# Performance work log

Measured on AMD Instinct MI355X. Metric: run time of the kernel, lower is better.

Reference implementation:

```python
import jax, jax.numpy as jnp
import numpy as np
import math

N = 20000          # nodes
E = 320000         # edges (avg degree 16)
NS, NV = 16, 4     # scalar / vector multiplicities
NCAT = 10
CAT_VOCAB = 119
DIST_DIM = 32
LIG_MAX_R = 5.0
W1_NUMEL = NS * NS + NS * NV          # 320 : layer1 tp weights
W2_NUMEL = NS * NS + NV * NS + NS * NV + NV * NV + NV * NV  # 416


def setup_inputs() -> dict:
    key = jax.random.key(0)
    ks = jax.random.split(key, 24)
    s = 0.1
    inp = {
        'x_cat': jax.random.randint(ks[0], (N, NCAT), 0, 2),
        'x_scalar': jax.random.normal(ks[1], (N, 32), jnp.float32),
        'pos': jax.random.normal(ks[2], (N, 3), jnp.float32) * 3.0,
        'edge_index': jax.random.randint(ks[3], (2, E), 0, N),
        'edge_bond': jax.random.uniform(ks[4], (E, 10), jnp.float32),
        # AtomEncoder params
        'emb_tables': jax.random.normal(ks[5], (NCAT, CAT_VOCAB, NS)) * s,
        'node_w': jax.random.normal(ks[6], (32, NS)) * s,
        'node_b': jnp.zeros((NS,), jnp.float32),
        # lig_edge_embedding MLP (42 -> ns -> ns)
        'em_w1': jax.random.normal(ks[7], (10 + DIST_DIM, NS)) * s,
        'em_b1': jnp.zeros((NS,), jnp.float32),
        'em_w2': jax.random.normal(ks[8], (NS, NS)) * s,
        'em_b2': jnp.zeros((NS,), jnp.float32),
        'c1_w1': jax.random.normal(ks[9], (3 * NS, 3 * NS)) * s,
        'c1_b1': jnp.zeros((3 * NS,), jnp.float32),
        'c1_w2': jax.random.normal(ks[10], (3 * NS, W1_NUMEL)) * s,
        'c1_b2': jnp.zeros((W1_NUMEL,), jnp.float32),
        # conv layer 2 fc
        'c2_w1': jax.random.normal(ks[11], (3 * NS, 3 * NS)) * s,
        'c2_b1': jnp.zeros((3 * NS,), jnp.float32),
        'c2_w2': jax.random.normal(ks[12], (3 * NS, W2_NUMEL)) * s,
        'c2_b2': jnp.zeros((W2_NUMEL,), jnp.float32),
    }
    return inp


def _scatter_mean(vals, idx, n):
    s = jax.ops.segment_sum(vals, idx, num_segments=n)
    cnt = jax.ops.segment_sum(jnp.ones(idx.shape, vals.dtype), idx, num_segments=n)
    return s / jnp.maximum(cnt, 1.0)[:, None]


def _forward(x_cat, x_scalar, pos, edge_index, edge_bond,
             emb_tables, node_w, node_b, em_w1, em_b1, em_w2, em_b2,
             c1_w1, c1_b1, c1_w2, c1_b2, c2_w1, c2_b1, c2_w2, c2_b2):
    ns, nv = NS, NV
    n = x_cat.shape[0]
    # ---- AtomEncoder: sum of categorical embeddings + linear(scalar) ----
    gathered = emb_tables[jnp.arange(NCAT)[None, :], x_cat]      # [N, 10, ns]
    node = gathered.sum(axis=1) + x_scalar @ node_w + node_b    # [N, ns]

    src, dst = edge_index[0], edge_index[1]
    vec = pos[dst] - pos[src]                                   # [E, 3]
    dist = jnp.sqrt(jnp.sum(vec * vec, axis=-1) + 1e-12)
    unit = vec / (dist + 1e-8)[:, None]
    # spherical harmonics, lmax=1, component normalization: [1, sqrt(3)*r_hat]
    sh0 = jnp.ones((vec.shape[0], 1), vec.dtype)
    sh1 = math.sqrt(3.0) * unit                                 # [E, 3]

    # ---- GaussianSmearing + edge embedding MLP ----
    offset = jnp.linspace(0.0, LIG_MAX_R, DIST_DIM)
    coeff = -0.5 / float(LIG_MAX_R / (DIST_DIM - 1)) ** 2
    demb = jnp.exp(coeff * (dist[:, None] - offset[None, :]) ** 2)
    e_in = jnp.concatenate([edge_bond, demb], axis=1)           # [E, 42]
    edge_emb = jax.nn.relu(e_in @ em_w1 + em_b1) @ em_w2 + em_b2  # [E, ns]

    # ======== conv layer 1: ns x0e -> ns x0e + nv x1o ========
    ea = jnp.concatenate([edge_emb, node[src, :ns], node[dst, :ns]], axis=1)
    w = jax.nn.relu(ea @ c1_w1 + c1_b1) @ c1_w2 + c1_b2         # [E, 320]
    wa = w[:, :ns * ns].reshape(-1, ns, ns)
    wb = w[:, ns * ns:].reshape(-1, ns, nv)
    s_dst = node[dst]                                           # [E, ns]
    a = 1.0 / math.sqrt(ns)                                     # fan-in norm
    out0 = jnp.einsum('euk,eu->ek', wa, s_dst) * sh0 * a        # 0e x 0e -> 0e
    out1 = jnp.einsum('euw,eu->ew', wb, s_dst)[:, :, None] * sh1[:, None, :] * a
    tp = jnp.concatenate([out0, out1.reshape(-1, 3 * nv)], axis=1)
    node = _scatter_mean(tp, src, n)                            # [N, ns+3nv]

    # ======== conv layer 2: ns x0e + nv x1o -> ns x0e + nv x1o + nv x1e ====
    ea = jnp.concatenate([edge_emb, node[src, :ns], node[dst, :ns]], axis=1)
    w = jax.nn.relu(ea @ c2_w1 + c2_b1) @ c2_w2 + c2_b2         # [E, 416]
    o = 0
    wa = w[:, o:o + ns * ns].reshape(-1, ns, ns); o += ns * ns
    wb = w[:, o:o + nv * ns].reshape(-1, nv, ns); o += nv * ns
    wc = w[:, o:o + ns * nv].reshape(-1, ns, nv); o += ns * nv
    wd = w[:, o:o + nv * nv].reshape(-1, nv, nv); o += nv * nv
    we = w[:, o:o + nv * nv].reshape(-1, nv, nv)
    s = node[dst, :ns]
    v = node[dst, ns:].reshape(-1, nv, 3)
    a0 = 1.0 / math.sqrt(ns + nv)   # two paths into 0e
    a1 = 1.0 / math.sqrt(ns + nv)   # two paths into 1o
    aE = 1.0 / math.sqrt(nv)        # one path into 1e
    vdot = jnp.einsum('evi,ei->ev', v, sh1)                     # 1o . 1o
    out0 = (jnp.einsum('euk,eu->ek', wa, s) * sh0
            + jnp.einsum('euk,eu->ek', wb, vdot) / math.sqrt(3.0)) * a0
    out1o = (jnp.einsum('euw,eu->ew', wc, s)[:, :, None] * sh1[:, None, :]
             + jnp.einsum('euw,eui->ewi', wd, v) * sh0[:, :, None]) * a1
    crossv = jnp.cross(v, jnp.broadcast_to(sh1[:, None, :], v.shape))
    out1e = jnp.einsum('euw,eui->ewi', we, crossv) * (aE / math.sqrt(2.0))
    tp = jnp.concatenate([out0, out1o.reshape(-1, 3 * nv),
                          out1e.reshape(-1, 3 * nv)], axis=1)
    node = _scatter_mean(tp, src, n)                            # [N, ns+6nv] = [N,40]
    return node


def reference(x_cat, x_scalar, pos, edge_index, edge_bond,
              emb_tables, node_w, node_b, em_w1, em_b1, em_w2, em_b2,
              c1_w1, c1_b1, c1_w2, c1_b2, c2_w1, c2_b1, c2_w2, c2_b2):
    return _forward(x_cat, x_scalar, pos, edge_index, edge_bond,
                    emb_tables, node_w, node_b, em_w1, em_b1, em_w2, em_b2,
                    c1_w1, c1_b1, c1_w2, c1_b2, c2_w1, c2_b1, c2_w2, c2_b2)
```

## Files before the change

kernel.cpp:

```cpp
#include <hip/hip_runtime.h>
#include <math.h>

#define NN 20000
#define NE 320000
#define NCPY 4

typedef _Float16 f16x8 __attribute__((ext_vector_type(8)));
typedef float f32x4 __attribute__((ext_vector_type(4)));
typedef unsigned short ushort_t;
typedef unsigned int uint_t;

#define MFMA16(A,B,C) __builtin_amdgcn_mfma_f32_16x16x32_f16((A),(B),(C),0,0,0)
#define LDS_FENCE() do{ asm volatile("s_waitcnt lgkmcnt(0)" ::: "memory"); __builtin_amdgcn_sched_barrier(0);}while(0)

static_assert(NE % 256 == 0, "edge grid must tile exactly");

__device__ __forceinline__ float frelu(float x){ return fmaxf(x, 0.0f); }

__device__ __forceinline__ void splitf(float x, ushort_t& h, ushort_t& l){
    _Float16 hh = (_Float16)x;
    float r = (x - (float)hh) * 2048.0f;
    _Float16 ll = (_Float16)r;
    union { _Float16 f; ushort_t u; } ch, cl;
    ch.f = hh; cl.f = ll;
    h = ch.u; l = cl.u;
}

__device__ __forceinline__ void edge_embed(
    int e, int s, int d,
    const float* __restrict__ pos,
    const float* __restrict__ edge_bond,
    const float* __restrict__ em_w1, const float* __restrict__ em_b1,
    const float* __restrict__ em_w2, const float* __restrict__ em_b2,
    float* eemb, float* sh1)
{
    float vx = pos[d*3+0] - pos[s*3+0];
    float vy = pos[d*3+1] - pos[s*3+1];
    float vz = pos[d*3+2] - pos[s*3+2];
    float d2 = vx*vx + vy*vy + vz*vz + 1e-12f;
    float dist = sqrtf(d2);
    float inv = 1.0f / (dist + 1e-8f);
    const float SQ3 = 1.7320508075688772f;
    sh1[0] = SQ3 * vx * inv;
    sh1[1] = SQ3 * vy * inv;
    sh1[2] = SQ3 * vz * inv;

    float ein[42];
    #pragma unroll
    for (int t = 0; t < 10; ++t) ein[t] = edge_bond[e*10 + t];
    const float coeff = -19.22f;
    const float step  = 5.0f / 31.0f;
    #pragma unroll
    for (int k = 0; k < 32; ++k) {
        float dd = dist - step * (float)k;
        ein[10+k] = __expf(coeff * dd * dd);
    }

    float t1[16];
    #pragma unroll
    for (int j = 0; j < 16; ++j) t1[j] = em_b1[j];
    #pragma unroll
    for (int t = 0; t < 42; ++t) {
        float v = ein[t];
        #pragma unroll
        for (int j = 0; j < 16; ++j) t1[j] += v * em_w1[t*16 + j];
    }
    #pragma unroll
    for (int j = 0; j < 16; ++j) t1[j] = frelu(t1[j]);

    #pragma unroll
    for (int j = 0; j < 16; ++j) eemb[j] = em_b2[j];
    #pragma unroll
    for (int t = 0; t < 16; ++t) {
        float v = t1[t];
        #pragma unroll
        for (int j = 0; j < 16; ++j) eemb[j] += v * em_w2[t*16 + j];
    }
}

__global__ __launch_bounds__(256)
void k_node_y(const float* __restrict__ node, int stride,
              const float* __restrict__ w1, float* __restrict__ y)
{
    int n = blockIdx.x*256 + threadIdx.x;
    if (n >= NN) return;
    float sv[16];
    const float4* r = reinterpret_cast<const float4*>(node + (size_t)n*stride);
    #pragma unroll
    for (int k = 0; k < 4; ++k) {
        float4 q = r[k];
        sv[4*k]=q.x; sv[4*k+1]=q.y; sv[4*k+2]=q.z; sv[4*k+3]=q.w;
    }
    float yb[48];
    #pragma unroll
    for (int j = 0; j < 48; ++j) yb[j] = 0.f;
    #pragma unroll
    for (int t = 0; t < 16; ++t) {
        float v = sv[t];
        #pragma unroll
        for (int j = 0; j < 48; ++j) yb[j] += v * w1[(16+t)*48 + j];
    }
    float* yo = y + (size_t)n*96;
    #pragma unroll
    for (int j = 0; j < 12; ++j)
        reinterpret_cast<float4*>(yo)[j] = make_float4(yb[4*j], yb[4*j+1], yb[4*j+2], yb[4*j+3]);
    #pragma unroll
    for (int j = 0; j < 48; ++j) yb[j] = 0.f;
    #pragma unroll
    for (int t = 0; t < 16; ++t) {
        float v = sv[t];
        #pragma unroll
        for (int j = 0; j < 48; ++j) yb[j] += v * w1[(32+t)*48 + j];
    }
    #pragma unroll
    for (int j = 0; j < 12; ++j)
        reinterpret_cast<float4*>(yo + 48)[j] = make_float4(yb[4*j], yb[4*j+1], yb[4*j+2], yb[4*j+3]);
}

__global__ __launch_bounds__(256)
void k_pack(const float* __restrict__ w2, const float* __restrict__ b2,
            ushort_t* __restrict__ out, int NC, int ntiles)
{
    int slot = blockIdx.x*256 + threadIdx.x;
    if (slot >= ntiles*128) return;
    int tl = slot >> 7; int r7 = slot & 127; int kb = r7 >> 6; int ll = r7 & 63;
    int col = tl*16 + (ll & 15);
    int k0 = (kb<<5) + ((ll>>4)<<3);
    uint_t hw[4], lw[4];
    #pragma unroll
    for (int p = 0; p < 4; ++p) {
        int ka = k0 + 2*p, kb2 = k0 + 2*p + 1;
        float va = (ka < 48) ? w2[ka*NC + col] : (ka == 48 ? b2[col] : 0.0f);
        float vb = (kb2 < 48) ? w2[kb2*NC + col] : (kb2 == 48 ? b2[col] : 0.0f);
        ushort_t ah, al, bh, bl;
        splitf(va, ah, al);
        splitf(vb, bh, bl);
        hw[p] = (uint_t)ah | ((uint_t)bh << 16);
        lw[p] = (uint_t)al | ((uint_t)bl << 16);
    }
    int base = tl*2048 + kb*1024 + ll*8;
    *reinterpret_cast<uint4*>(&out[base])       = make_uint4(hw[0], hw[1], hw[2], hw[3]);
    *reinterpret_cast<uint4*>(&out[base + 512]) = make_uint4(lw[0], lw[1], lw[2], lw[3]);
}

struct B4 { f16x8 h0, l0, h1, l1; };
__device__ __forceinline__ B4 loadB(const f16x8* __restrict__ g, int t, int l) {
    B4 b;
    const f16x8* p = g + t*256 + l;
    b.h0 = p[0];
    b.l0 = p[64];
    b.h1 = p[128];
    b.l1 = p[192];
    return b;
}

__device__ __forceinline__ void stage_A(ushort_t* bounce, int l,
                                        const uint_t* hph, const uint_t* hpl,
                                        f16x8 ahi[4][2], f16x8 alo[4][2])
{
    #pragma unroll
    for (int t = 0; t < 4; ++t)
        *reinterpret_cast<uint4*>(&bounce[l*32 + t*8]) = make_uint4(0,0,0,0);
    LDS_FENCE();
    #pragma unroll
    for (int mt = 0; mt < 4; ++mt) {
        if ((l >> 4) == mt) {
            #pragma unroll
            for (int jj = 0; jj < 25; ++jj) {
                int k = jj*2, kb = k >> 5, kk = k & 31;
                int lr = (l & 15) + ((kk >> 3) << 4);
                int off = kb*512 + lr*8 + (kk & 7);
                *reinterpret_cast<uint_t*>(&bounce[off])        = hph[jj];
                *reinterpret_cast<uint_t*>(&bounce[1024 + off]) = hpl[jj];
            }
        }
        LDS_FENCE();
        ahi[mt][0] = *reinterpret_cast<const f16x8*>(&bounce[l*8]);
        ahi[mt][1] = *reinterpret_cast<const f16x8*>(&bounce[512 + l*8]);
        alo[mt][0] = *reinterpret_cast<const f16x8*>(&bounce[1024 + l*8]);
        alo[mt][1] = *reinterpret_cast<const f16x8*>(&bounce[1536 + l*8]);
        LDS_FENCE();
    }
}

__device__ __forceinline__ void build_h_reg(
    const float* em, int s, int d,
    const float* __restrict__ y,
    const float* __restrict__ w1, const float* __restrict__ b1,
    float* h)
{
    #pragma unroll
    for (int j = 0; j < 48; ++j) h[j] = b1[j];
    #pragma unroll
    for (int t = 0; t < 16; ++t) {
        float v = em[t];
        #pragma unroll
        for (int j = 0; j < 48; ++j) h[j] += v * w1[t*48 + j];
    }
    const float4* pb = reinterpret_cast<const float4*>(y + (size_t)s*96);
    const float4* pc = reinterpret_cast<const float4*>(y + (size_t)d*96 + 48);
    #pragma unroll
    for (int kk = 0; kk < 12; ++kk) {
        float4 qb = pb[kk], qc = pc[kk];
        h[4*kk+0] = frelu(h[4*kk+0] + qb.x + qc.x);
        h[4*kk+1] = frelu(h[4*kk+1] + qb.y + qc.y);
        h[4*kk+2] = frelu(h[4*kk+2] + qb.z + qc.z);
        h[4*kk+3] = frelu(h[4*kk+3] + qb.w + qc.w);
    }
}

__global__ __launch_bounds__(256)
void k_node_feat(const int* __restrict__ x_cat, const float* __restrict__ x_scalar,
                 const float* __restrict__ emb, const float* __restrict__ node_w,
                 const float* __restrict__ node_b, float* __restrict__ node0)
{
    int n = blockIdx.x * 256 + threadIdx.x;
    if (n >= NN) return;
    float acc[16];
    #pragma unroll
    for (int k = 0; k < 16; ++k) acc[k] = node_b[k];
    #pragma unroll
    for (int c = 0; c < 10; ++c) {
        int idx = x_cat[n*10 + c];
        const float4* row = reinterpret_cast<const float4*>(emb + (c*119 + idx)*16);
        #pragma unroll
        for (int k = 0; k < 4; ++k) {
            float4 q = row[k];
            acc[4*k+0] += q.x; acc[4*k+1] += q.y; acc[4*k+2] += q.z; acc[4*k+3] += q.w;
        }
    }
    #pragma unroll
    for (int t = 0; t < 32; ++t) {
        float xs = x_scalar[n*32 + t];
        #pragma unroll
        for (int k = 0; k < 16; ++k) acc[k] += xs * node_w[t*16 + k];
    }
    #pragma unroll
    for (int k = 0; k < 16; ++k) node0[n*16 + k] = acc[k];
}

__global__ __launch_bounds__(256)
void k_edge_l1(const int* __restrict__ ei, const float* __restrict__ pos,
               const float* __restrict__ edge_bond,
               const float* __restrict__ em_w1, const float* __restrict__ em_b1,
               const float* __restrict__ em_w2, const float* __restrict__ em_b2,
               const float* __restrict__ w1, const float* __restrict__ b1,
               const ushort_t* __restrict__ packW,
               const float* __restrict__ y,
               const float* __restrict__ node0,
               float* __restrict__ eembG, float* __restrict__ eshG,
               float* __restrict__ accumC, float* __restrict__ cnt)
{
    __shared__ __align__(16) unsigned char smem[20736];
    float* sT  = (float*)smem;
    float* sSh = (float*)(smem + 16640);
    int*   sSrc= (int*)(smem + 19712);

    int tid = threadIdx.x;
    int l = tid & 63;
    int cc = l & 15;
    int e = blockIdx.x*256 + tid;
    int s = ei[e], d = ei[NE + e];
    float* __restrict__ accum = accumC + (size_t)(blockIdx.x & (NCPY-1)) * (NN*28);

    float em[16], sh1[3];
    edge_embed(e, s, d, pos, edge_bond, em_w1, em_b1, em_w2, em_b2, em, sh1);
    {
        float4* pe = reinterpret_cast<float4*>(eembG + (size_t)e*16);
        #pragma unroll
        for (int k = 0; k < 4; ++k)
            pe[k] = make_float4(em[4*k], em[4*k+1], em[4*k+2], em[4*k+3]);
        reinterpret_cast<float4*>(eshG)[e] = make_float4(sh1[0], sh1[1], sh1[2], 0.f);
    }
    atomicAdd(cnt + s, 1.0f);

    float sd[16];
    {
        const float4* rd = reinterpret_cast<const float4*>(node0 + (size_t)d*16);
        #pragma unroll
        for (int k = 0; k < 4; ++k) {
            float4 q = rd[k];
            sd[4*k]=q.x; sd[4*k+1]=q.y; sd[4*k+2]=q.z; sd[4*k+3]=q.w;
        }
    }
    float h[48];
    build_h_reg(em, s, d, y, w1, b1, h);

    uint_t hph[25], hpl[25];
    #pragma unroll
    for (int jj = 0; jj < 24; ++jj) {
        ushort_t ah, al, bh, bl;
        splitf(h[2*jj],   ah, al);
        splitf(h[2*jj+1], bh, bl);
        hph[jj] = (uint_t)ah | ((uint_t)bh << 16);
        hpl[jj] = (uint_t)al | ((uint_t)bl << 16);
    }
    hph[24] = 0x3C00u;
    hpl[24] = 0u;

    f16x8 ahi[4][2], alo[4][2];
    stage_A((ushort_t*)smem + (tid >> 6)*2048, l, hph, hpl, ahi, alo);

    __syncthreads();
    sSrc[tid] = s;
    #pragma unroll
    for (int u = 0; u < 16; ++u) sT[u*260 + tid] = sd[u];
    sSh[tid*3+0] = sh1[0]; sSh[tid*3+1] = sh1[1]; sSh[tid*3+2] = sh1[2];
    __syncthreads();

    f32x4 out0[4];
    float ob[4][4];
    #pragma unroll
    for (int mt = 0; mt < 4; ++mt) {
        out0[mt] = (f32x4){0.f,0.f,0.f,0.f};
        #pragma unroll
        for (int r = 0; r < 4; ++r) ob[mt][r] = 0.f;
    }

    const f16x8* gB = reinterpret_cast<const f16x8*>(packW);

    auto process = [&](int t, const B4& cur) {
        #pragma unroll
        for (int mt = 0; mt < 4; ++mt) {
            f32x4 Dh = (f32x4){0.f,0.f,0.f,0.f};
            f32x4 Dc = (f32x4){0.f,0.f,0.f,0.f};
            Dh = MFMA16(ahi[mt][0], cur.h0, Dh);
            Dh = MFMA16(ahi[mt][1], cur.h1, Dh);
            Dc = MFMA16(alo[mt][0], cur.h0, Dc);
            Dc = MFMA16(ahi[mt][0], cur.l0, Dc);
            Dc = MFMA16(alo[mt][1], cur.h1, Dc);
            Dc = MFMA16(ahi[mt][1], cur.l1, Dc);
            f32x4 D = Dh + Dc * 0.00048828125f;
            int elb = (tid & 192) + (mt << 4) + ((l >> 4) << 2);
            if (t < 16) {
                f32x4 sv = *reinterpret_cast<const f32x4*>(&sT[t*260 + elb]);
                out0[mt] += sv * D;
            } else {
                const float* sp = &sT[(((t-16)<<2) + (cc>>2))*260 + elb];
                #pragma unroll
                for (int r = 0; r < 4; ++r) ob[mt][r] += sp[r] * D[r];
            }
        }
    };

    B4 b0 = loadB(gB, 0, l), b1v = loadB(gB, 1, l);
    #pragma unroll 1
    for (int t = 0; t < 20; t += 2) {
        B4 p0 = (t + 2 < 20) ? loadB(gB, t + 2, l) : b0;
        process(t, b0);
        B4 p1 = (t + 3 < 20) ? loadB(gB, t + 3, l) : b1v;
        process(t + 1, b1v);
        b0 = p0; b1v = p1;
    }

    #pragma unroll
    for (int mt = 0; mt < 4; ++mt) {
        int elb = (tid & 192) + (mt << 4) + ((l >> 4) << 2);
        #pragma unroll
        for (int r = 0; r < 4; ++r) {
            int el = elb + r;
            int sidx = sSrc[el];
            atomicAdd(accum + (size_t)sidx*28 + cc, out0[mt][r] * 0.25f);
            float x = ob[mt][r];
            x += __shfl_xor(x, 4); x += __shfl_xor(x, 8);
            int q = cc / 3; int i = cc - q*3;
            float xq = __shfl(x, (l & 48) | q);
            if (cc < 12)
                atomicAdd(accum + (size_t)sidx*28 + 16 + cc, 0.25f * xq * sSh[el*3 + i]);
        }
    }
}

__global__ __launch_bounds__(256)
void k_edge_l2(const int* __restrict__ ei,
               const float* __restrict__ w1, const float* __restrict__ b1,
               const ushort_t* __restrict__ packW,
               const float* __restrict__ eembG, const float* __restrict__ eshG,
               const float* __restrict__ y,
               const float* __restrict__ node1,
               float* __restrict__ accumC)
{
    __shared__ __align__(16) unsigned char smem[37376];
    float* sT  = (float*)smem;
    float* sVd = (float*)(smem + 16640);
    float* sV  = (float*)(smem + 20800);
    float* sSh = (float*)(smem + 33280);
    int*   sSrc= (int*)(smem + 36352);

    int tid = threadIdx.x;
    int l = tid & 63;
    int cc = l & 15;
    int e = blockIdx.x*256 + tid;
    int s = ei[e], d = ei[NE + e];
    float* __restrict__ accum2 = accumC + (size_t)(blockIdx.x & (NCPY-1)) * (NN*40);

    float4 shv = reinterpret_cast<const float4*>(eshG)[e];
    float sh1[3] = {shv.x, shv.y, shv.z};
    float sd[16], vv[12];
    {
        const float4* rd = reinterpret_cast<const float4*>(node1 + (size_t)d*28);
        #pragma unroll
        for (int k = 0; k < 4; ++k) {
            float4 q = rd[k];
            sd[4*k]=q.x; sd[4*k+1]=q.y; sd[4*k+2]=q.z; sd[4*k+3]=q.w;
        }
        #pragma unroll
        for (int k = 0; k < 3; ++k) {
            float4 q = rd[4+k];
            vv[4*k]=q.x; vv[4*k+1]=q.y; vv[4*k+2]=q.z; vv[4*k+3]=q.w;
        }
    }
    float vdr[4];
    const float INV_SQ3 = 0.5773502691896258f;
    #pragma unroll
    for (int u = 0; u < 4; ++u)
        vdr[u] = (vv[u*3]*sh1[0] + vv[u*3+1]*sh1[1] + vv[u*3+2]*sh1[2]) * INV_SQ3;

    float em[16];
    {
        const float4* pe = reinterpret_cast<const float4*>(eembG + (size_t)e*16);
        #pragma unroll
        for (int k = 0; k < 4; ++k) {
            float4 q = pe[k];
            em[4*k]=q.x; em[4*k+1]=q.y; em[4*k+2]=q.z; em[4*k+3]=q.w;
        }
    }
    float h[48];
    build_h_reg(em, s, d, y, w1, b1, h);

    uint_t hph[25], hpl[25];
    #pragma unroll
    for (int jj = 0; jj < 24; ++jj) {
        ushort_t ah, al, bh, bl;
        splitf(h[2*jj],   ah, al);
        splitf(h[2*jj+1], bh, bl);
        hph[jj] = (uint_t)ah | ((uint_t)bh << 16);
        hpl[jj] = (uint_t)al | ((uint_t)bl << 16);
    }
    hph[24] = 0x3C00u;
    hpl[24] = 0u;

    f16x8 ahi[4][2], alo[4][2];
    stage_A((ushort_t*)smem + (tid >> 6)*2048, l, hph, hpl, ahi, alo);

    __syncthreads();
    sSrc[tid] = s;
    #pragma unroll
    for (int u = 0; u < 16; ++u) sT[u*260 + tid] = sd[u];
    #pragma unroll
    for (int u = 0; u < 4; ++u) sVd[u*260 + tid] = vdr[u];
    #pragma unroll
    for (int k = 0; k < 12; ++k) sV[k*260 + tid] = vv[k];
    sSh[tid*3+0] = sh1[0]; sSh[tid*3+1] = sh1[1]; sSh[tid*3+2] = sh1[2];
    __syncthreads();

    const float A0 = 0.22360679774997896f;
    const float AE = 0.3535533905932738f;

    f32x4 out0[4];
    float outc[4][4];
    #pragma unroll
    for (int mt = 0; mt < 4; ++mt) {
        out0[mt] = (f32x4){0.f,0.f,0.f,0.f};
        #pragma unroll
        for (int r = 0; r < 4; ++r) outc[mt][r] = 0.f;
    }

    const f16x8* gB = reinterpret_cast<const f16x8*>(packW);

    auto process = [&](int t, const B4& cur) {
        #pragma unroll
        for (int mt = 0; mt < 4; ++mt) {
            f32x4 Dh = (f32x4){0.f,0.f,0.f,0.f};
            f32x4 Dc = (f32x4){0.f,0.f,0.f,0.f};
            Dh = MFMA16(ahi[mt][0], cur.h0, Dh);
            Dh = MFMA16(ahi[mt][1], cur.h1, Dh);
            Dc = MFMA16(alo[mt][0], cur.h0, Dc);
            Dc = MFMA16(ahi[mt][0], cur.l0, Dc);
            Dc = MFMA16(alo[mt][1], cur.h1, Dc);
            Dc = MFMA16(ahi[mt][1], cur.l1, Dc);
            f32x4 D = Dh + Dc * 0.00048828125f;
            int elb = (tid & 192) + (mt << 4) + ((l >> 4) << 2);
            if (t < 16) {
                f32x4 sv = *reinterpret_cast<const f32x4*>(&sT[t*260 + elb]);
                out0[mt] += sv * D;
            } else if (t < 20) {
                f32x4 vd = *reinterpret_cast<const f32x4*>(&sVd[(t-16)*260 + elb]);
                out0[mt] += vd * D;
            } else if (t < 24) {
                const float* sp = &sT[(((t-20)<<2) + (cc>>2))*260 + elb];
                #pragma unroll
                for (int r = 0; r < 4; ++r) outc[mt][r] += sp[r] * D[r];
            } else if (t == 24) {
                int base3 = (cc >> 2) * 3;
                #pragma unroll
                for (int r = 0; r < 4; ++r) {
                    int el = elb + r;
                    float vx = sV[(base3+0)*260 + el];
                    float vy = sV[(base3+1)*260 + el];
                    float vz = sV[(base3+2)*260 + el];
                    float a0 = D[r]*vx, a1 = D[r]*vy, a2 = D[r]*vz;
                    a0 += __shfl_xor(a0,4); a0 += __shfl_xor(a0,8);
                    a1 += __shfl_xor(a1,4); a1 += __shfl_xor(a1,8);
                    a2 += __shfl_xor(a2,4); a2 += __shfl_xor(a2,8);
                    float xc = outc[mt][r];
                    xc += __shfl_xor(xc,4); xc += __shfl_xor(xc,8);
                    int q = cc / 3; int i = cc - q*3;
                    int srcl = (l & 48) | q;
                    float g0 = __shfl(a0, srcl), g1 = __shfl(a1, srcl), g2 = __shfl(a2, srcl);
                    float oo = (i==0) ? g0 : ((i==1) ? g1 : g2);
                    float xq = __shfl(xc, srcl);
                    if (cc < 12) {
                        float sh1i = sSh[el*3 + i];
                        atomicAdd(accum2 + (size_t)sSrc[el]*40 + 16 + cc,
                                  A0 * (xq * sh1i + oo));
                    }
                }
            } else {
                int base3 = (cc >> 2) * 3;
                #pragma unroll
                for (int r = 0; r < 4; ++r) {
                    int el = elb + r;
                    float vx = sV[(base3+0)*260 + el];
                    float vy = sV[(base3+1)*260 + el];
                    float vz = sV[(base3+2)*260 + el];
                    float sx = sSh[el*3+0], sy = sSh[el*3+1], sz = sSh[el*3+2];
                    float cx = vy*sz - vz*sy;
                    float cy = vz*sx - vx*sz;
                    float cz = vx*sy - vy*sx;
                    float a0 = D[r]*cx, a1 = D[r]*cy, a2 = D[r]*cz;
                    a0 += __shfl_xor(a0,4); a0 += __shfl_xor(a0,8);
                    a1 += __shfl_xor(a1,4); a1 += __shfl_xor(a1,8);
                    a2 += __shfl_xor(a2,4); a2 += __shfl_xor(a2,8);
                    int q = cc / 3; int i = cc - q*3;
                    int srcl = (l & 48) | q;
                    float g0 = __shfl(a0, srcl), g1 = __shfl(a1, srcl), g2 = __shfl(a2, srcl);
                    float oo = (i==0) ? g0 : ((i==1) ? g1 : g2);
                    if (cc < 12)
                        atomicAdd(accum2 + (size_t)sSrc[el]*40 + 28 + cc, AE * oo);
                }
            }
        }
    };

    B4 b0 = loadB(gB, 0, l), b1v = loadB(gB, 1, l);
    #pragma unroll 1
    for (int t = 0; t < 26; t += 2) {
        B4 p0 = (t + 2 < 26) ? loadB(gB, t + 2, l) : b0;
        process(t, b0);
        B4 p1 = (t + 3 < 26) ? loadB(gB, t + 3, l) : b1v;
        process(t + 1, b1v);
        b0 = p0; b1v = p1;
    }

    #pragma unroll
    for (int mt = 0; mt < 4; ++mt) {
        int elb = (tid & 192) + (mt << 4) + ((l >> 4) << 2);
        #pragma unroll
        for (int r = 0; r < 4; ++r) {
            int el = elb + r;
            atomicAdd(accum2 + (size_t)sSrc[el]*40 + cc, out0[mt][r] * A0);
        }
    }
}

__global__ __launch_bounds__(256)
void k_divm(const float* __restrict__ in, int stride, float* __restrict__ out,
            const float* __restrict__ cnt, int cols, int total)
{
    int i = blockIdx.x * 256 + threadIdx.x;
    if (i >= total) return;
    int n = i / cols;
    float sum = 0.f;
    #pragma unroll
    for (int c = 0; c < NCPY; ++c) sum += in[(size_t)c*stride + i];
    out[i] = sum / fmaxf(cnt[n], 1.0f);
}

extern "C" void kernel_launch(void* const* d_in, const int* in_sizes, int n_in,
                              void* d_out, int out_size, void* d_ws, size_t ws_size,
                              hipStream_t stream) {
    const int*   x_cat     = (const int*)  d_in[0];
    const float* x_scalar  = (const float*)d_in[1];
    const float* pos       = (const float*)d_in[2];
    const int*   ei        = (const int*)  d_in[3];
    const float* edge_bond = (const float*)d_in[4];
    const float* emb       = (const float*)d_in[5];
    const float* node_w    = (const float*)d_in[6];
    const float* node_b    = (const float*)d_in[7];
    const float* em_w1     = (const float*)d_in[8];
    const float* em_b1     = (const float*)d_in[9];
    const float* em_w2     = (const float*)d_in[10];
    const float* em_b2     = (const float*)d_in[11];
    const float* c1_w1     = (const float*)d_in[12];
    const float* c1_b1     = (const float*)d_in[13];
    const float* c1_w2     = (const float*)d_in[14];
    const float* c1_b2     = (const float*)d_in[15];
    const float* c2_w1     = (const float*)d_in[16];
    const float* c2_b1     = (const float*)d_in[17];
    const float* c2_w2     = (const float*)d_in[18];
    const float* c2_b2     = (const float*)d_in[19];

    float* ws    = (float*)d_ws;
    float* node0 = ws;
    float* cnt   = ws + 320000;
    ushort_t* packA = (ushort_t*)(ws + 340000);
    ushort_t* packB = packA + 20*2048;
    float* eembG = ws + 400000;
    float* eshG  = ws + 5520000;
    float* yBuf  = ws + 6800000;
    float* node1 = ws + 8720000;
    float* accumC= ws + 9280000;

    hipMemsetAsync(cnt, 0, 20000 * sizeof(float), stream);
    hipMemsetAsync(accumC, 0, (size_t)NCPY * NN * 28 * sizeof(float), stream);

    k_pack<<<(20*128 + 255) / 256, 256, 0, stream>>>(c1_w2, c1_b2, packA, 320, 20);
    k_pack<<<(26*128 + 255) / 256, 256, 0, stream>>>(c2_w2, c2_b2, packB, 416, 26);

    k_node_feat<<<(NN + 255) / 256, 256, 0, stream>>>(
        x_cat, x_scalar, emb, node_w, node_b, node0);

    k_node_y<<<(NN + 255) / 256, 256, 0, stream>>>(node0, 16, c1_w1, yBuf);

    k_edge_l1<<<NE / 256, 256, 0, stream>>>(
        ei, pos, edge_bond, em_w1, em_b1, em_w2, em_b2,
        c1_w1, c1_b1, packA, yBuf, node0, eembG, eshG, accumC, cnt);

    k_divm<<<(560000 + 255) / 256, 256, 0, stream>>>(accumC, NN*28, node1, cnt, 28, 560000);

    hipMemsetAsync(accumC, 0, (size_t)NCPY * NN * 40 * sizeof(float), stream);

    k_node_y<<<(NN + 255) / 256, 256, 0, stream>>>(node1, 28, c2_w1, yBuf);

    k_edge_l2<<<NE / 256, 256, 0, stream>>>(
        ei, c2_w1, c2_b1, packB, eembG, eshG, yBuf, node1, accumC);

    k_divm<<<(800000 + 255) / 256, 256, 0, stream>>>(accumC, NN*40, (float*)d_out, cnt, 40, 800000);
}
```

Baseline: 333.2 us.

## Replace atomic scatter-mean with CSR sort by source and segmented gather

Builds a CSR ordering of edges by source node (degree count, single-block scan, atomic scatter into a permutation). The edge kernels then process edges in that sorted order and write per-edge tensor-product rows densely instead of doing float atomics into four replicated accumulators. A gather kernel sums each node's contiguous rows and divides by degree. This removes atomic contention and the memsets and reduction passes, but adds three preprocessing kernels (one a single-block serial scan), a large per-edge intermediate buffer, and indirect, less coalesced edge input reads through perm.

```diff
diff --git a/kernel.cpp b/kernel.cpp
--- a/kernel.cpp
+++ b/kernel.cpp
@@ -3,7 +3,6 @@
 
 #define NN 20000
 #define NE 320000
-#define NCPY 4
 
 typedef _Float16 f16x8 __attribute__((ext_vector_type(8)));
 typedef float f32x4 __attribute__((ext_vector_type(4)));
@@ -79,6 +78,47 @@
 }
 
 __global__ __launch_bounds__(256)
+void k_deg(const int* __restrict__ ei, int* __restrict__ deg)
+{
+    int e = blockIdx.x*256 + threadIdx.x;
+    if (e < NE) atomicAdd(&deg[ei[e]], 1);
+}
+
+__global__ __launch_bounds__(256)
+void k_scan(const int* __restrict__ deg, int* __restrict__ rowptr, int* __restrict__ off)
+{
+    __shared__ int part[256];
+    int t = threadIdx.x;
+    const int chunk = (NN + 255) / 256;
+    int lo = t*chunk, hi = lo + chunk; if (hi > NN) hi = NN; if (lo > NN) lo = NN;
+    int s = 0;
+    for (int i = lo; i < hi; ++i) s += deg[i];
+    part[t] = s;
+    __syncthreads();
+    for (int ofs = 1; ofs < 256; ofs <<= 1) {
+        int v = (t >= ofs) ? part[t-ofs] : 0;
+        __syncthreads();
+        part[t] += v;
+        __syncthreads();
+    }
+    int run = (t == 0) ? 0 : part[t-1];
+    for (int i = lo; i < hi; ++i) {
+        rowptr[i] = run; off[i] = run;
+        run += deg[i];
+    }
+    if (t == 255) rowptr[NN] = NE;
+}
+
+__global__ __launch_bounds__(256)
+void k_scatter(const int* __restrict__ ei, int* __restrict__ off, int* __restrict__ perm)
+{
+    int e = blockIdx.x*256 + threadIdx.x;
+    if (e >= NE) return;
+    int p = atomicAdd(&off[ei[e]], 1);
+    perm[p] = e;
+}
+
+__global__ __launch_bounds__(256)
 void k_node_y(const float* __restrict__ node, int stride,
               const float* __restrict__ w1, float* __restrict__ y)
 {
@@ -248,31 +288,31 @@
                const ushort_t* __restrict__ packW,
                const float* __restrict__ y,
                const float* __restrict__ node0,
+               const int* __restrict__ perm,
                float* __restrict__ eembG, float* __restrict__ eshG,
-               float* __restrict__ accumC, float* __restrict__ cnt)
+               float* __restrict__ tp)
 {
     __shared__ __align__(16) unsigned char smem[20736];
     float* sT  = (float*)smem;
     float* sSh = (float*)(smem + 16640);
-    int*   sSrc= (int*)(smem + 19712);
 
     int tid = threadIdx.x;
     int l = tid & 63;
     int cc = l & 15;
-    int e = blockIdx.x*256 + tid;
+    int i = blockIdx.x*256 + tid;
+    int e = perm[i];
     int s = ei[e], d = ei[NE + e];
-    float* __restrict__ accum = accumC + (size_t)(blockIdx.x & (NCPY-1)) * (NN*28);
+    size_t rowbase = (size_t)blockIdx.x * 256;
 
     float em[16], sh1[3];
     edge_embed(e, s, d, pos, edge_bond, em_w1, em_b1, em_w2, em_b2, em, sh1);
     {
-        float4* pe = reinterpret_cast<float4*>(eembG + (size_t)e*16);
+        float4* pe = reinterpret_cast<float4*>(eembG + (size_t)i*16);
         #pragma unroll
         for (int k = 0; k < 4; ++k)
             pe[k] = make_float4(em[4*k], em[4*k+1], em[4*k+2], em[4*k+3]);
-        reinterpret_cast<float4*>(eshG)[e] = make_float4(sh1[0], sh1[1], sh1[2], 0.f);
-    }
-    atomicAdd(cnt + s, 1.0f);
+        reinterpret_cast<float4*>(eshG)[i] = make_float4(sh1[0], sh1[1], sh1[2], 0.f);
+    }
 
     float sd[16];
     {
@@ -302,7 +342,6 @@
     stage_A((ushort_t*)smem + (tid >> 6)*2048, l, hph, hpl, ahi, alo);
 
     __syncthreads();
-    sSrc[tid] = s;
     #pragma unroll
     for (int u = 0; u < 16; ++u) sT[u*260 + tid] = sd[u];
     sSh[tid*3+0] = sh1[0]; sSh[tid*3+1] = sh1[1]; sSh[tid*3+2] = sh1[2];
@@ -359,14 +398,14 @@
         #pragma unroll
         for (int r = 0; r < 4; ++r) {
             int el = elb + r;
-            int sidx = sSrc[el];
-            atomicAdd(accum + (size_t)sidx*28 + cc, out0[mt][r] * 0.25f);
+            float* row = tp + (rowbase + el)*28;
+            row[cc] = out0[mt][r] * 0.25f;
             float x = ob[mt][r];
             x += __shfl_xor(x, 4); x += __shfl_xor(x, 8);
-            int q = cc / 3; int i = cc - q*3;
+            int q = cc / 3; int i2 = cc - q*3;
             float xq = __shfl(x, (l & 48) | q);
             if (cc < 12)
-                atomicAdd(accum + (size_t)sidx*28 + 16 + cc, 0.25f * xq * sSh[el*3 + i]);
+                row[16 + cc] = 0.25f * xq * sSh[el*3 + i2];
         }
     }
 }
@@ -378,23 +417,24 @@
                const float* __restrict__ eembG, const float* __restrict__ eshG,
                const float* __restrict__ y,
                const float* __restrict__ node1,
-               float* __restrict__ accumC)
-{
-    __shared__ __align__(16) unsigned char smem[37376];
+               const int* __restrict__ perm,
+               float* __restrict__ tp)
+{
+    __shared__ __align__(16) unsigned char smem[36352];
     float* sT  = (float*)smem;
     float* sVd = (float*)(smem + 16640);
     float* sV  = (float*)(smem + 20800);
     float* sSh = (float*)(smem + 33280);
-    int*   sSrc= (int*)(smem + 36352);
 
     int tid = threadIdx.x;
     int l = tid & 63;
     int cc = l & 15;
-    int e = blockIdx.x*256 + tid;
+    int i = blockIdx.x*256 + tid;
+    int e = perm[i];
     int s = ei[e], d = ei[NE + e];
-    float* __restrict__ accum2 = accumC + (size_t)(blockIdx.x & (NCPY-1)) * (NN*40);
-
-    float4 shv = reinterpret_cast<const float4*>(eshG)[e];
+    size_t rowbase = (size_t)blockIdx.x * 256;
+
+    float4 shv = reinterpret_cast<const float4*>(eshG)[i];
     float sh1[3] = {shv.x, shv.y, shv.z};
     float sd[16], vv[12];
     {
@@ -418,7 +458,7 @@
 
     float em[16];
     {
-        const float4* pe = reinterpret_cast<const float4*>(eembG + (size_t)e*16);
+        const float4* pe = reinterpret_cast<const float4*>(eembG + (size_t)i*16);
         #pragma unroll
         for (int k = 0; k < 4; ++k) {
             float4 q = pe[k];
@@ -444,7 +484,6 @@
     stage_A((ushort_t*)smem + (tid >> 6)*2048, l, hph, hpl, ahi, alo);
 
     __syncthreads();
-    sSrc[tid] = s;
     #pragma unroll
     for (int u = 0; u < 16; ++u) sT[u*260 + tid] = sd[u];
     #pragma unroll
@@ -505,15 +544,14 @@
                     a2 += __shfl_xor(a2,4); a2 += __shfl_xor(a2,8);
                     float xc = outc[mt][r];
                     xc += __shfl_xor(xc,4); xc += __shfl_xor(xc,8);
-                    int q = cc / 3; int i = cc - q*3;
+                    int q = cc / 3; int i2 = cc - q*3;
                     int srcl = (l & 48) | q;
                     float g0 = __shfl(a0, srcl), g1 = __shfl(a1, srcl), g2 = __shfl(a2, srcl);
-                    float oo = (i==0) ? g0 : ((i==1) ? g1 : g2);
+                    float oo = (i2==0) ? g0 : ((i2==1) ? g1 : g2);
                     float xq = __shfl(xc, srcl);
                     if (cc < 12) {
-                        float sh1i = sSh[el*3 + i];
-                        atomicAdd(accum2 + (size_t)sSrc[el]*40 + 16 + cc,
-                                  A0 * (xq * sh1i + oo));
+                        float sh1i = sSh[el*3 + i2];
+                        tp[(rowbase + el)*40 + 16 + cc] = A0 * (xq * sh1i + oo);
                     }
                 }
             } else {
@@ -532,12 +570,12 @@
                     a0 += __shfl_xor(a0,4); a0 += __shfl_xor(a0,8);
                     a1 += __shfl_xor(a1,4); a1 += __shfl_xor(a1,8);
                     a2 += __shfl_xor(a2,4); a2 += __shfl_xor(a2,8);
-                    int q = cc / 3; int i = cc - q*3;
+                    int q = cc / 3; int i2 = cc - q*3;
                     int srcl = (l & 48) | q;
                     float g0 = __shfl(a0, srcl), g1 = __shfl(a1, srcl), g2 = __shfl(a2, srcl);
-                    float oo = (i==0) ? g0 : ((i==1) ? g1 : g2);
+                    float oo = (i2==0) ? g0 : ((i2==1) ? g1 : g2);
                     if (cc < 12)
-                        atomicAdd(accum2 + (size_t)sSrc[el]*40 + 28 + cc, AE * oo);
+                        tp[(rowbase + el)*40 + 28 + cc] = AE * oo;
                 }
             }
         }
@@ -559,22 +597,32 @@
         #pragma unroll
         for (int r = 0; r < 4; ++r) {
             int el = elb + r;
-            atomicAdd(accum2 + (size_t)sSrc[el]*40 + cc, out0[mt][r] * A0);
-        }
-    }
-}
-
-__global__ __launch_bounds__(256)
-void k_divm(const float* __restrict__ in, int stride, float* __restrict__ out,
-            const float* __restrict__ cnt, int cols, int total)
-{
-    int i = blockIdx.x * 256 + threadIdx.x;
-    if (i >= total) return;
-    int n = i / cols;
-    float sum = 0.f;
-    #pragma unroll
-    for (int c = 0; c < NCPY; ++c) sum += in[(size_t)c*stride + i];
-    out[i] = sum / fmaxf(cnt[n], 1.0f);
+            tp[(rowbase + el)*40 + cc] = out0[mt][r] * A0;
+        }
+    }
+}
+
+template<int C>
+__global__ __launch_bounds__(256)
+void k_gather(const float* __restrict__ tp, const int* __restrict__ rowptr,
+              float* __restrict__ out)
+{
+    int i = blockIdx.x*256 + threadIdx.x;
+    if (i >= NN*C) return;
+    int n = i / C; int c = i - n*C;
+    int r0 = rowptr[n], r1 = rowptr[n+1];
+    float s0=0.f, s1=0.f, s2=0.f, s3=0.f;
+    int r = r0;
+    for (; r + 4 <= r1; r += 4) {
+        s0 += tp[(size_t)(r+0)*C + c];
+        s1 += tp[(size_t)(r+1)*C + c];
+        s2 += tp[(size_t)(r+2)*C + c];
+        s3 += tp[(size_t)(r+3)*C + c];
+    }
+    for (; r < r1; ++r) s0 += tp[(size_t)r*C + c];
+    float sum = (s0 + s1) + (s2 + s3);
+    float inv = (r1 > r0) ? 1.0f / (float)(r1 - r0) : 1.0f;
+    out[i] = sum * inv;
 }
 
 extern "C" void kernel_launch(void* const* d_in, const int* in_sizes, int n_in,
@@ -603,17 +651,23 @@
 
     float* ws    = (float*)d_ws;
     float* node0 = ws;
-    float* cnt   = ws + 320000;
-    ushort_t* packA = (ushort_t*)(ws + 340000);
+    float* node1 = ws + 320000;
+    int*   degI  = (int*)(ws + 880000);
+    int*   rowp  = (int*)(ws + 900000);
+    int*   offI  = (int*)(ws + 920008);
+    int*   permI = (int*)(ws + 940008);
+    ushort_t* packA = (ushort_t*)(ws + 1260008);
     ushort_t* packB = packA + 20*2048;
-    float* eembG = ws + 400000;
-    float* eshG  = ws + 5520000;
-    float* yBuf  = ws + 6800000;
-    float* node1 = ws + 8720000;
-    float* accumC= ws + 9280000;
-
-    hipMemsetAsync(cnt, 0, 20000 * sizeof(float), stream);
-    hipMemsetAsync(accumC, 0, (size_t)NCPY * NN * 28 * sizeof(float), stream);
+    float* eembG = ws + 1307112;
+    float* eshG  = ws + 6427112;
+    float* yBuf  = ws + 7707112;
+    float* tp    = ws + 9627112;
+
+    hipMemsetAsync(degI, 0, 20000 * sizeof(int), stream);
+
+    k_deg<<<(NE + 255) / 256, 256, 0, stream>>>(ei, degI);
+    k_scan<<<1, 256, 0, stream>>>(degI, rowp, offI);
+    k_scatter<<<(NE + 255) / 256, 256, 0, stream>>>(ei, offI, permI);
 
     k_pack<<<(20*128 + 255) / 256, 256, 0, stream>>>(c1_w2, c1_b2, packA, 320, 20);
     k_pack<<<(26*128 + 255) / 256, 256, 0, stream>>>(c2_w2, c2_b2, packB, 416, 26);
@@ -625,16 +679,14 @@
 
     k_edge_l1<<<NE / 256, 256, 0, stream>>>(
         ei, pos, edge_bond, em_w1, em_b1, em_w2, em_b2,
-        c1_w1, c1_b1, packA, yBuf, node0, eembG, eshG, accumC, cnt);
-
-    k_divm<<<(560000 + 255) / 256, 256, 0, stream>>>(accumC, NN*28, node1, cnt, 28, 560000);
-
-    hipMemsetAsync(accumC, 0, (size_t)NCPY * NN * 40 * sizeof(float), stream);
+        c1_w1, c1_b1, packA, yBuf, node0, permI, eembG, eshG, tp);
+
+    k_gather<28><<<(NN*28 + 255) / 256, 256, 0, stream>>>(tp, rowp, node1);
 
     k_node_y<<<(NN + 255) / 256, 256, 0, stream>>>(node1, 28, c2_w1, yBuf);
 
     k_edge_l2<<<NE / 256, 256, 0, stream>>>(
-        ei, c2_w1, c2_b1, packB, eembG, eshG, yBuf, node1, accumC);
-
-    k_divm<<<(800000 + 255) / 256, 256, 0, stream>>>(accumC, NN*40, (float*)d_out, cnt, 40, 800000);
-}
+        ei, c2_w1, c2_b1, packB, eembG, eshG, yBuf, node1, permI, tp);
+
+    k_gather<40><<<(NN*40 + 255) / 256, 256, 0, stream>>>(tp, rowp, (float*)d_out);
+}
```

Measured after the change: 424.3 us. +27.3%, slower.

## Use single-wave edge blocks with LDS fences and drop replicated accumulators

Applied to the files above, without the earlier changes.

Edge kernels now launch 64-thread blocks, one wavefront each, so __syncthreads is replaced by LDS waitcnt fences and the shared memory per block shrinks. The four-way replicated atomic accumulation buffers are removed: atomics go to a single accumulator, and the divide kernels no longer sum copies. The memsets are merged into one. The aim is to cut barrier cost and LDS pressure and raise occupancy, at the cost of more atomic contention on one buffer.

```diff
diff --git a/kernel.cpp b/kernel.cpp
--- a/kernel.cpp
+++ b/kernel.cpp
@@ -3,7 +3,6 @@
 
 #define NN 20000
 #define NE 320000
-#define NCPY 4
 
 typedef _Float16 f16x8 __attribute__((ext_vector_type(8)));
 typedef float f32x4 __attribute__((ext_vector_type(4)));
@@ -13,7 +12,7 @@
 #define MFMA16(A,B,C) __builtin_amdgcn_mfma_f32_16x16x32_f16((A),(B),(C),0,0,0)
 #define LDS_FENCE() do{ asm volatile("s_waitcnt lgkmcnt(0)" ::: "memory"); __builtin_amdgcn_sched_barrier(0);}while(0)
 
-static_assert(NE % 256 == 0, "edge grid must tile exactly");
+static_assert(NE % 64 == 0, "edge grid must tile exactly");
 
 __device__ __forceinline__ float frelu(float x){ return fmaxf(x, 0.0f); }
 
@@ -239,7 +238,7 @@
     for (int k = 0; k < 16; ++k) node0[n*16 + k] = acc[k];
 }
 
-__global__ __launch_bounds__(256)
+__global__ __launch_bounds__(64)
 void k_edge_l1(const int* __restrict__ ei, const float* __restrict__ pos,
                const float* __restrict__ edge_bond,
                const float* __restrict__ em_w1, const float* __restrict__ em_b1,
@@ -249,19 +248,17 @@
                const float* __restrict__ y,
                const float* __restrict__ node0,
                float* __restrict__ eembG, float* __restrict__ eshG,
-               float* __restrict__ accumC, float* __restrict__ cnt)
-{
-    __shared__ __align__(16) unsigned char smem[20736];
+               float* __restrict__ accum, float* __restrict__ cnt)
+{
+    __shared__ __align__(16) unsigned char smem[5376];
     float* sT  = (float*)smem;
-    float* sSh = (float*)(smem + 16640);
-    int*   sSrc= (int*)(smem + 19712);
-
-    int tid = threadIdx.x;
-    int l = tid & 63;
+    float* sSh = (float*)(smem + 4352);
+    int*   sSrc= (int*)(smem + 5120);
+
+    int l = threadIdx.x;
     int cc = l & 15;
-    int e = blockIdx.x*256 + tid;
+    int e = blockIdx.x*64 + l;
     int s = ei[e], d = ei[NE + e];
-    float* __restrict__ accum = accumC + (size_t)(blockIdx.x & (NCPY-1)) * (NN*28);
 
     float em[16], sh1[3];
     edge_embed(e, s, d, pos, edge_bond, em_w1, em_b1, em_w2, em_b2, em, sh1);
@@ -299,14 +296,14 @@
     hpl[24] = 0u;
 
     f16x8 ahi[4][2], alo[4][2];
-    stage_A((ushort_t*)smem + (tid >> 6)*2048, l, hph, hpl, ahi, alo);
-
-    __syncthreads();
-    sSrc[tid] = s;
-    #pragma unroll
-    for (int u = 0; u < 16; ++u) sT[u*260 + tid] = sd[u];
-    sSh[tid*3+0] = sh1[0]; sSh[tid*3+1] = sh1[1]; sSh[tid*3+2] = sh1[2];
-    __syncthreads();
+    stage_A((ushort_t*)smem, l, hph, hpl, ahi, alo);
+
+    LDS_FENCE();
+    sSrc[l] = s;
+    #pragma unroll
+    for (int u = 0; u < 16; ++u) sT[u*68 + l] = sd[u];
+    sSh[l*3+0] = sh1[0]; sSh[l*3+1] = sh1[1]; sSh[l*3+2] = sh1[2];
+    LDS_FENCE();
 
     f32x4 out0[4];
     float ob[4][4];
@@ -331,12 +328,12 @@
             Dc = MFMA16(alo[mt][1], cur.h1, Dc);
             Dc = MFMA16(ahi[mt][1], cur.l1, Dc);
             f32x4 D = Dh + Dc * 0.00048828125f;
-            int elb = (tid & 192) + (mt << 4) + ((l >> 4) << 2);
+            int elb = (mt << 4) + ((l >> 4) << 2);
             if (t < 16) {
-                f32x4 sv = *reinterpret_cast<const f32x4*>(&sT[t*260 + elb]);
+                f32x4 sv = *reinterpret_cast<const f32x4*>(&sT[t*68 + elb]);
                 out0[mt] += sv * D;
             } else {
-                const float* sp = &sT[(((t-16)<<2) + (cc>>2))*260 + elb];
+                const float* sp = &sT[(((t-16)<<2) + (cc>>2))*68 + elb];
                 #pragma unroll
                 for (int r = 0; r < 4; ++r) ob[mt][r] += sp[r] * D[r];
             }
@@ -355,7 +352,7 @@
 
     #pragma unroll
     for (int mt = 0; mt < 4; ++mt) {
-        int elb = (tid & 192) + (mt << 4) + ((l >> 4) << 2);
+        int elb = (mt << 4) + ((l >> 4) << 2);
         #pragma unroll
         for (int r = 0; r < 4; ++r) {
             int el = elb + r;
@@ -363,36 +360,34 @@
             atomicAdd(accum + (size_t)sidx*28 + cc, out0[mt][r] * 0.25f);
             float x = ob[mt][r];
             x += __shfl_xor(x, 4); x += __shfl_xor(x, 8);
-            int q = cc / 3; int i = cc - q*3;
+            int q = cc / 3; int i2 = cc - q*3;
             float xq = __shfl(x, (l & 48) | q);
             if (cc < 12)
-                atomicAdd(accum + (size_t)sidx*28 + 16 + cc, 0.25f * xq * sSh[el*3 + i]);
-        }
-    }
-}
-
-__global__ __launch_bounds__(256)
+                atomicAdd(accum + (size_t)sidx*28 + 16 + cc, 0.25f * xq * sSh[el*3 + i2]);
+        }
+    }
+}
+
+__global__ __launch_bounds__(64)
 void k_edge_l2(const int* __restrict__ ei,
                const float* __restrict__ w1, const float* __restrict__ b1,
                const ushort_t* __restrict__ packW,
                const float* __restrict__ eembG, const float* __restrict__ eshG,
                const float* __restrict__ y,
                const float* __restrict__ node1,
-               float* __restrict__ accumC)
-{
-    __shared__ __align__(16) unsigned char smem[37376];
+               float* __restrict__ accum2)
+{
+    __shared__ __align__(16) unsigned char smem[9728];
     float* sT  = (float*)smem;
-    float* sVd = (float*)(smem + 16640);
-    float* sV  = (float*)(smem + 20800);
-    float* sSh = (float*)(smem + 33280);
-    int*   sSrc= (int*)(smem + 36352);
-
-    int tid = threadIdx.x;
-    int l = tid & 63;
+    float* sVd = (float*)(smem + 4352);
+    float* sV  = (float*)(smem + 5440);
+    float* sSh = (float*)(smem + 8704);
+    int*   sSrc= (int*)(smem + 9472);
+
+    int l = threadIdx.x;
     int cc = l & 15;
-    int e = blockIdx.x*256 + tid;
+    int e = blockIdx.x*64 + l;
     int s = ei[e], d = ei[NE + e];
-    float* __restrict__ accum2 = accumC + (size_t)(blockIdx.x & (NCPY-1)) * (NN*40);
 
     float4 shv = reinterpret_cast<const float4*>(eshG)[e];
     float sh1[3] = {shv.x, shv.y, shv.z};
@@ -441,18 +436,18 @@
     hpl[24] = 0u;
 
     f16x8 ahi[4][2], alo[4][2];
-    stage_A((ushort_t*)smem + (tid >> 6)*2048, l, hph, hpl, ahi, alo);
-
-    __syncthreads();
-    sSrc[tid] = s;
-    #pragma unroll
-    for (int u = 0; u < 16; ++u) sT[u*260 + tid] = sd[u];
-    #pragma unroll
-    for (int u = 0; u < 4; ++u) sVd[u*260 + tid] = vdr[u];
-    #pragma unroll
-    for (int k = 0; k < 12; ++k) sV[k*260 + tid] = vv[k];
-    sSh[tid*3+0] = sh1[0]; sSh[tid*3+1] = sh1[1]; sSh[tid*3+2] = sh1[2];
-    __syncthreads();
+    stage_A((ushort_t*)smem, l, hph, hpl, ahi, alo);
+
+    LDS_FENCE();
+    sSrc[l] = s;
+    #pragma unroll
+    for (int u = 0; u < 16; ++u) sT[u*68 + l] = sd[u];
+    #pragma unroll
+    for (int u = 0; u < 4; ++u) sVd[u*68 + l] = vdr[u];
+    #pragma unroll
+    for (int k = 0; k < 12; ++k) sV[k*68 + l] = vv[k];
+    sSh[l*3+0] = sh1[0]; sSh[l*3+1] = sh1[1]; sSh[l*3+2] = sh1[2];
+    LDS_FENCE();
 
     const float A0 = 0.22360679774997896f;
     const float AE = 0.3535533905932738f;
@@ -480,15 +475,15 @@
             Dc = MFMA16(alo[mt][1], cur.h1, Dc);
             Dc = MFMA16(ahi[mt][1], cur.l1, Dc);
             f32x4 D = Dh + Dc * 0.00048828125f;
-            int elb = (tid & 192) + (mt << 4) + ((l >> 4) << 2);
+            int elb = (mt << 4) + ((l >> 4) << 2);
             if (t < 16) {
-                f32x4 sv = *reinterpret_cast<const f32x4*>(&sT[t*260 + elb]);
+                f32x4 sv = *reinterpret_cast<const f32x4*>(&sT[t*68 + elb]);
                 out0[mt] += sv * D;
             } else if (t < 20) {
-                f32x4 vd = *reinterpret_cast<const f32x4*>(&sVd[(t-16)*260 + elb]);
+                f32x4 vd = *reinterpret_cast<const f32x4*>(&sVd[(t-16)*68 + elb]);
                 out0[mt] += vd * D;
             } else if (t < 24) {
-                const float* sp = &sT[(((t-20)<<2) + (cc>>2))*260 + elb];
+                const float* sp = &sT[(((t-20)<<2) + (cc>>2))*68 + elb];
                 #pragma unroll
                 for (int r = 0; r < 4; ++r) outc[mt][r] += sp[r] * D[r];
             } else if (t == 24) {
@@ -496,22 +491,22 @@
                 #pragma unroll
                 for (int r = 0; r < 4; ++r) {
                     int el = elb + r;
-                    float vx = sV[(base3+0)*260 + el];
-                    float vy = sV[(base3+1)*260 + el];
-                    float vz = sV[(base3+2)*260 + el];
+                    float vx = sV[(base3+0)*68 + el];
+                    float vy = sV[(base3+1)*68 + el];
+                    float vz = sV[(base3+2)*68 + el];
                     float a0 = D[r]*vx, a1 = D[r]*vy, a2 = D[r]*vz;
                     a0 += __shfl_xor(a0,4); a0 += __shfl_xor(a0,8);
                     a1 += __shfl_xor(a1,4); a1 += __shfl_xor(a1,8);
                     a2 += __shfl_xor(a2,4); a2 += __shfl_xor(a2,8);
                     float xc = outc[mt][r];
                     xc += __shfl_xor(xc,4); xc += __shfl_xor(xc,8);
-                    int q = cc / 3; int i = cc - q*3;
+                    int q = cc / 3; int i2 = cc - q*3;
                     int srcl = (l & 48) | q;
                     float g0 = __shfl(a0, srcl), g1 = __shfl(a1, srcl), g2 = __shfl(a2, srcl);
-                    float oo = (i==0) ? g0 : ((i==1) ? g1 : g2);
+                    float oo = (i2==0) ? g0 : ((i2==1) ? g1 : g2);
                     float xq = __shfl(xc, srcl);
                     if (cc < 12) {
-                        float sh1i = sSh[el*3 + i];
+                        float sh1i = sSh[el*3 + i2];
                         atomicAdd(accum2 + (size_t)sSrc[el]*40 + 16 + cc,
                                   A0 * (xq * sh1i + oo));
                     }
@@ -521,9 +516,9 @@
                 #pragma unroll
                 for (int r = 0; r < 4; ++r) {
                     int el = elb + r;
-                    float vx = sV[(base3+0)*260 + el];
-                    float vy = sV[(base3+1)*260 + el];
-                    float vz = sV[(base3+2)*260 + el];
+                    float vx = sV[(base3+0)*68 + el];
+                    float vy = sV[(base3+1)*68 + el];
+                    float vz = sV[(base3+2)*68 + el];
                     float sx = sSh[el*3+0], sy = sSh[el*3+1], sz = sSh[el*3+2];
                     float cx = vy*sz - vz*sy;
                     float cy = vz*sx - vx*sz;
@@ -532,10 +527,10 @@
                     a0 += __shfl_xor(a0,4); a0 += __shfl_xor(a0,8);
                     a1 += __shfl_xor(a1,4); a1 += __shfl_xor(a1,8);
                     a2 += __shfl_xor(a2,4); a2 += __shfl_xor(a2,8);
-                    int q = cc / 3; int i = cc - q*3;
+                    int q = cc / 3; int i2 = cc - q*3;
                     int srcl = (l & 48) | q;
                     float g0 = __shfl(a0, srcl), g1 = __shfl(a1, srcl), g2 = __shfl(a2, srcl);
-                    float oo = (i==0) ? g0 : ((i==1) ? g1 : g2);
+                    float oo = (i2==0) ? g0 : ((i2==1) ? g1 : g2);
                     if (cc < 12)
                         atomicAdd(accum2 + (size_t)sSrc[el]*40 + 28 + cc, AE * oo);
                 }
@@ -555,7 +550,7 @@
 
     #pragma unroll
     for (int mt = 0; mt < 4; ++mt) {
-        int elb = (tid & 192) + (mt << 4) + ((l >> 4) << 2);
+        int elb = (mt << 4) + ((l >> 4) << 2);
         #pragma unroll
         for (int r = 0; r < 4; ++r) {
             int el = elb + r;
@@ -565,16 +560,13 @@
 }
 
 __global__ __launch_bounds__(256)
-void k_divm(const float* __restrict__ in, int stride, float* __restrict__ out,
-            const float* __restrict__ cnt, int cols, int total)
+void k_div(const float* __restrict__ in, float* __restrict__ out,
+           const float* __restrict__ cnt, int cols, int total)
 {
     int i = blockIdx.x * 256 + threadIdx.x;
     if (i >= total) return;
     int n = i / cols;
-    float sum = 0.f;
-    #pragma unroll
-    for (int c = 0; c < NCPY; ++c) sum += in[(size_t)c*stride + i];
-    out[i] = sum / fmaxf(cnt[n], 1.0f);
+    out[i] = in[i] / fmaxf(cnt[n], 1.0f);
 }
 
 extern "C" void kernel_launch(void* const* d_in, const int* in_sizes, int n_in,
@@ -603,17 +595,17 @@
 
     float* ws    = (float*)d_ws;
     float* node0 = ws;
-    float* cnt   = ws + 320000;
-    ushort_t* packA = (ushort_t*)(ws + 340000);
+    float* accum1= ws + 320000;
+    float* accum2= ws + 880000;
+    float* cnt   = ws + 1680000;
+    float* node1 = ws + 1700000;
+    ushort_t* packA = (ushort_t*)(ws + 2260000);
     ushort_t* packB = packA + 20*2048;
-    float* eembG = ws + 400000;
-    float* eshG  = ws + 5520000;
-    float* yBuf  = ws + 6800000;
-    float* node1 = ws + 8720000;
-    float* accumC= ws + 9280000;
-
-    hipMemsetAsync(cnt, 0, 20000 * sizeof(float), stream);
-    hipMemsetAsync(accumC, 0, (size_t)NCPY * NN * 28 * sizeof(float), stream);
+    float* eembG = ws + 2307104;
+    float* eshG  = ws + 7427104;
+    float* yBuf  = ws + 8707104;
+
+    hipMemsetAsync(accum1, 0, (size_t)(560000 + 800000 + 20000) * sizeof(float), stream);
 
     k_pack<<<(20*128 + 255) / 256, 256, 0, stream>>>(c1_w2, c1_b2, packA, 320, 20);
     k_pack<<<(26*128 + 255) / 256, 256, 0, stream>>>(c2_w2, c2_b2, packB, 416, 26);
@@ -623,18 +615,16 @@
 
     k_node_y<<<(NN + 255) / 256, 256, 0, stream>>>(node0, 16, c1_w1, yBuf);
 
-    k_edge_l1<<<NE / 256, 256, 0, stream>>>(
+    k_edge_l1<<<NE / 64, 64, 0, stream>>>(
         ei, pos, edge_bond, em_w1, em_b1, em_w2, em_b2,
-        c1_w1, c1_b1, packA, yBuf, node0, eembG, eshG, accumC, cnt);
-
-    k_divm<<<(560000 + 255) / 256, 256, 0, stream>>>(accumC, NN*28, node1, cnt, 28, 560000);
-
-    hipMemsetAsync(accumC, 0, (size_t)NCPY * NN * 40 * sizeof(float), stream);
+        c1_w1, c1_b1, packA, yBuf, node0, eembG, eshG, accum1, cnt);
+
+    k_div<<<(560000 + 255) / 256, 256, 0, stream>>>(accum1, node1, cnt, 28, 560000);
 
     k_node_y<<<(NN + 255) / 256, 256, 0, stream>>>(node1, 28, c2_w1, yBuf);
 
-    k_edge_l2<<<NE / 256, 256, 0, stream>>>(
-        ei, c2_w1, c2_b1, packB, eembG, eshG, yBuf, node1, accumC);
-
-    k_divm<<<(800000 + 255) / 256, 256, 0, stream>>>(accumC, NN*40, (float*)d_out, cnt, 40, 800000);
-}
+    k_edge_l2<<<NE / 64, 64, 0, stream>>>(
+        ei, c2_w1, c2_b1, packB, eembG, eshG, yBuf, node1, accum2);
+
+    k_div<<<(800000 + 255) / 256, 256, 0, stream>>>(accum2, (float*)d_out, cnt, 40, 800000);
+}
```

New measurement: 330.8 us, median of 2. No clear change (-0.7%).
